# Kernel optimization log

Hardware: AMD Instinct MI355X
Metric: run time of the kernel (lower is better)

## Reference

```python
import jax, jax.numpy as jnp
import numpy as np

B, L = 32, 200
NUM_C, NUM_D, DIM_V = 256, 32, 128


def setup_inputs() -> dict:
    key = jax.random.key(0)
    ks = jax.random.split(key, 20)
    def n(k, shape, s=0.05):
        return (jax.random.normal(k, shape) * s).astype(jnp.float32)
    return {
        "c_seq": jax.random.randint(ks[0], (B, L), 0, NUM_C),
        "d_seq": jax.random.randint(ks[1], (B, L), 0, NUM_D),
        "r_seq": jax.random.uniform(ks[2], (B, L), dtype=jnp.float32),
        # learned params
        "X": n(ks[3], (NUM_C * NUM_D, DIM_V), 0.1),      # Embedding table
        "v_r": n(ks[4], (DIM_V,), 0.1),
        "v_beta": n(ks[5], (DIM_V,), 0.1),
        # GRU (torch layout: gates [r|z|n] stacked)
        "W_ih": n(ks[6], (3 * DIM_V, 2 * DIM_V)),
        "W_hh": n(ks[7], (3 * DIM_V, DIM_V)),
        "b_ih": n(ks[8], (3 * DIM_V,)),
        "b_hh": n(ks[9], (3 * DIM_V,)),
        # linear_1: dim_v -> dim_v -> num_d (dropout = identity in eval)
        "W1a": n(ks[10], (DIM_V, DIM_V)), "b1a": n(ks[11], (DIM_V,)),
        "W1b": n(ks[12], (NUM_D, DIM_V)), "b1b": n(ks[13], (NUM_D,)),
        # linear_2: 3*dim_v -> dim_v -> num_d
        "W2a": n(ks[14], (DIM_V, 3 * DIM_V)), "b2a": n(ks[15], (DIM_V,)),
        "W2b": n(ks[16], (NUM_D, DIM_V)), "b2b": n(ks[17], (NUM_D,)),
    }


def reference(c_seq, d_seq, r_seq, X, v_r, v_beta, W_ih, W_hh, b_ih, b_hh,
              W1a, b1a, W1b, b1b, W2a, b2a, W2b, b2b):
    # embedding lookup: x = c + num_c * d
    v_x_seq = X[c_seq + NUM_C * d_seq]              # [B,L,V]
    v_r_seq = r_seq[..., None] * v_r                # [B,L,V]
    gru_in = jnp.concatenate([v_x_seq, v_r_seq], -1)  # [B,L,2V]

    # GRU (torch semantics), precompute input projections
    gx = jnp.einsum('blf,gf->blg', gru_in, W_ih) + b_ih  # [B,L,3V]

    def gru_step(h, gx_t):
        gh = h @ W_hh.T + b_hh
        xr, xz, xn = jnp.split(gx_t, 3, axis=-1)
        hr, hz, hn = jnp.split(gh, 3, axis=-1)
        r = jax.nn.sigmoid(xr + hr)
        z = jax.nn.sigmoid(xz + hz)
        n_ = jnp.tanh(xn + r * hn)
        h = (1.0 - z) * n_ + z * h
        return h, h

    h0 = jnp.zeros((B, DIM_V), dtype=gru_in.dtype)
    _, h_seq = jax.lax.scan(gru_step, h0, jnp.swapaxes(gx, 0, 1))
    h_seq = jnp.swapaxes(h_seq, 0, 1)               # [B,L,V]

    # linear_1 (dropout is identity at inference)
    alpha_seq = jax.nn.relu(h_seq @ W1a.T + b1a) @ W1b.T + b1b  # [B,L,num_d]

    # sequential memory update; one-hot gather/scatter expressed as true
    # gather C[b, c_t, d_t] and row scatter C[b, c_t, :] = new_c (same math)
    bidx = jnp.arange(B)

    def mem_step(C, inp):
        c_t, d_t, vx_t, vr_t = inp
        beta = C[bidx, c_t, d_t]                    # [B]
        v_beta_t = beta[:, None] * v_beta           # [B,V]
        zcat = jnp.concatenate([v_beta_t, vx_t, vr_t], -1)  # [B,3V]
        new_c = jax.nn.relu(zcat @ W2a.T + b2a) @ W2b.T + b2b  # [B,num_d]
        C = C.at[bidx, c_t].set(new_c)
        return C, C

    C0 = jnp.zeros((B, NUM_C, NUM_D), jnp.float32)
    _, C_seq = jax.lax.scan(
        mem_step, C0,
        (jnp.swapaxes(c_seq, 0, 1), jnp.swapaxes(d_seq, 0, 1),
         jnp.swapaxes(v_x_seq, 0, 1), jnp.swapaxes(v_r_seq, 0, 1)))
    C_seq = jnp.swapaxes(C_seq, 0, 1)               # [B,L,num_c,num_d]
    return alpha_seq, h_seq, C_seq
```

## Files before the change

kernel.cpp:

```cpp
#include <hip/hip_runtime.h>
#include <hip/hip_bf16.h>

typedef unsigned short u16;
typedef unsigned int u32;
typedef short short8 __attribute__((ext_vector_type(8)));
typedef float f32x4 __attribute__((ext_vector_type(4)));

constexpr int BATCH = 32, L = 200, NUM_C = 256, NUM_D = 32, V = 128;
constexpr int G3 = 384;
constexpr int KQ = 512;
constexpr int ROWS = BATCH * L;
constexpr int TP = 208;
constexpr size_t ALPHA_OFF = 0;
constexpr size_t H_OFF = (size_t)ROWS * NUM_D;
constexpr size_t C_OFF = H_OFF + (size_t)ROWS * V;

__device__ inline u16 f2bf(float f) {
  __hip_bfloat16 h = __float2bfloat16(f);
  return __builtin_bit_cast(u16, h);
}
__device__ inline float bf2f(u16 u) { u32 x = ((u32)u) << 16; return __builtin_bit_cast(float, x); }

__device__ inline void cvt32(const float* __restrict__ src, u16* __restrict__ dst) {
#pragma unroll
  for (int j0 = 0; j0 < 32; j0 += 4) {
    const f32x4 v = *(const f32x4*)(src + j0);
    ushort4 s;
    s.x = f2bf(v[0]); s.y = f2bf(v[1]); s.z = f2bf(v[2]); s.w = f2bf(v[3]);
    *(ushort4*)(dst + j0) = s;
  }
}
__device__ inline short8 ldfrag(const float* __restrict__ p) {
  const f32x4 a = *(const f32x4*)p, b = *(const f32x4*)(p + 4);
  short8 s;
  s[0] = (short)f2bf(a[0]); s[1] = (short)f2bf(a[1]);
  s[2] = (short)f2bf(a[2]); s[3] = (short)f2bf(a[3]);
  s[4] = (short)f2bf(b[0]); s[5] = (short)f2bf(b[1]);
  s[6] = (short)f2bf(b[2]); s[7] = (short)f2bf(b[3]);
  return s;
}

__global__ __launch_bounds__(256) void k1(
    const int* __restrict__ c_seq, const int* __restrict__ d_seq,
    const float* __restrict__ r_seq, const float* __restrict__ X,
    const float* __restrict__ v_r, const float* __restrict__ W_ih,
    const float* __restrict__ W2a, const float* __restrict__ b_ih,
    const float* __restrict__ b2a, float* __restrict__ Qout)
{
  __shared__ __align__(16) u16 Als[64][144];
  __shared__ __align__(16) u16 Bls[64][144];
  const int tid = threadIdx.x;
  const int mt = blockIdx.x, nt = blockIdx.y;
  const int lane = tid & 63, w = tid >> 6;
  const int q = lane >> 4, m = lane & 15;

  f32x4 acc[4];
#pragma unroll
  for (int i = 0; i < 4; ++i) acc[i] = (f32x4)0.0f;

  const int r0 = tid >> 2;
  const int kc = (tid & 3) * 32;
  const int rowg = mt * 64 + r0;
  const int gcolB = nt * 64 + r0;

  for (int s = 0; s < 2; ++s) {
    if (s) __syncthreads();
    if (s == 0) {
      const int idx = c_seq[rowg] + NUM_C * d_seq[rowg];
      cvt32(X + (size_t)idx * V + kc, &Als[r0][kc]);
    } else {
      const float rv = r_seq[rowg];
#pragma unroll
      for (int j0 = 0; j0 < 32; j0 += 4) {
        const f32x4 v = *(const f32x4*)(v_r + kc + j0);
        ushort4 sv;
        sv.x = f2bf(rv * v[0]); sv.y = f2bf(rv * v[1]);
        sv.z = f2bf(rv * v[2]); sv.w = f2bf(rv * v[3]);
        *(ushort4*)&Als[r0][kc + j0] = sv;
      }
    }
    {
      const float* src = (gcolB < G3)
        ? (W_ih + (size_t)gcolB * 256 + s * 128 + kc)
        : (W2a + (size_t)(gcolB - G3) * G3 + V + s * 128 + kc);
      cvt32(src, &Bls[r0][kc]);
    }
    __syncthreads();
#pragma unroll
    for (int c = 0; c < 4; ++c) {
      const short8 af = *(const short8*)&Als[w * 16 + m][32 * c + 8 * q];
#pragma unroll
      for (int i = 0; i < 4; ++i) {
        const short8 bf = *(const short8*)&Bls[i * 16 + m][32 * c + 8 * q];
        acc[i] = __builtin_amdgcn_mfma_f32_16x16x32_bf16(af, bf, acc[i], 0, 0, 0);
      }
    }
  }
#pragma unroll
  for (int i = 0; i < 4; ++i) {
    const int col = nt * 64 + i * 16 + m;
    const float bias = (col < G3) ? b_ih[col] : b2a[col - G3];
#pragma unroll
    for (int r = 0; r < 4; ++r) {
      const int rowo = mt * 64 + w * 16 + q * 4 + r;
      Qout[(size_t)rowo * KQ + col] = acc[i][r] + bias;
    }
  }
}

union ShK2 {
  struct { u16 h_bf[2][V]; } g;
  struct {
    int cb[TP]; int db[TP]; int sp[TP];
    float nr[TP][36];
    float u[V];
    int maxd;
  } s;
};

__global__ __launch_bounds__(256, 1) void k2(
    const int* __restrict__ c_seq, const int* __restrict__ d_seq,
    const float* __restrict__ W_hh, const float* __restrict__ b_hh,
    const float* __restrict__ W2a, const float* __restrict__ v_beta,
    const float* __restrict__ W2b, const float* __restrict__ b2b,
    const float* __restrict__ Q, float* __restrict__ out)
{
  __shared__ __align__(16) ShK2 sh;
  const int tid = threadIdx.x;
  const int l = tid & 63, w = tid >> 6, q = l >> 4, m = l & 15;

  if (blockIdx.x < 32) {
    const int b = blockIdx.x;
    if (tid < V) sh.g.h_bf[0][tid] = 0;
    __syncthreads();
    short8 wf[6][4];
    float bhh[6]; int gcol[6];
#pragma unroll
    for (int i = 0; i < 6; ++i) {
      const int g = (w + 4 * i) * 16 + m;
      gcol[i] = g;
      bhh[i] = b_hh[g];
#pragma unroll
      for (int c = 0; c < 4; ++c)
        wf[i][c] = ldfrag(W_hh + (size_t)g * V + 32 * c + 8 * q);
    }
    const float* Qb = Q + (size_t)b * L * KQ;
    float* outh = out + H_OFF + (size_t)b * L * V;
    const int vi0 = 16 * w + m, vi1 = 64 + 16 * w + m;
    float hold[2] = {0.f, 0.f};
    float hst[2] = {0.f, 0.f};
    const f32x4 z4 = (f32x4)0.0f;
    float gxA[6], gxB[6];
#pragma unroll
    for (int i = 0; i < 6; ++i) gxA[i] = Qb[gcol[i]];
#pragma unroll
    for (int i = 0; i < 6; ++i) gxB[i] = Qb[KQ + gcol[i]];

    auto step = [&](int t, float (&gx)[6]) {
      const int rs = t & 1, wsl = rs ^ 1;
      short8 af[4];
#pragma unroll
      for (int c = 0; c < 4; ++c)
        af[c] = *(const short8*)&sh.g.h_bf[rs][32 * c + 8 * q];
      if (t > 0 && q == 0) {
        outh[(size_t)(t - 1) * V + vi0] = hst[0];
        outh[(size_t)(t - 1) * V + vi1] = hst[1];
      }
      f32x4 acc[6];
#pragma unroll
      for (int i = 0; i < 6; ++i)
        acc[i] = __builtin_amdgcn_mfma_f32_16x16x32_bf16(af[0], wf[i][0], z4, 0, 0, 0);
#pragma unroll
      for (int c = 1; c < 4; ++c)
#pragma unroll
        for (int i = 0; i < 6; ++i)
          acc[i] = __builtin_amdgcn_mfma_f32_16x16x32_bf16(af[c], wf[i][c], acc[i], 0, 0, 0);
      float hnew[2];
#pragma unroll
      for (int s = 0; s < 2; ++s) {
        const float xr = gx[0 + s] + acc[0 + s][0] + bhh[0 + s];
        const float xz = gx[2 + s] + acc[2 + s][0] + bhh[2 + s];
        const float ghn = acc[4 + s][0] + bhh[4 + s];
        const float r = 1.f / (1.f + __expf(-xr));
        const float z = 1.f / (1.f + __expf(-xz));
        const float xn = gx[4 + s] + r * ghn;
        const float e = __expf(2.f * xn);
        const float n = 1.f - 2.f / (e + 1.f);
        hnew[s] = (1.f - z) * n + z * hold[s];
      }
      if (q == 0) {
        sh.g.h_bf[wsl][vi0] = f2bf(hnew[0]);
        sh.g.h_bf[wsl][vi1] = f2bf(hnew[1]);
      }
      hold[0] = hnew[0]; hold[1] = hnew[1];
      hst[0] = hnew[0]; hst[1] = hnew[1];
      if (t + 2 < L) {
        const float* Qr = Qb + (size_t)(t + 2) * KQ;
#pragma unroll
        for (int i = 0; i < 6; ++i) gx[i] = Qr[gcol[i]];
      }
      __builtin_amdgcn_s_waitcnt(0xc07f);
      __builtin_amdgcn_s_barrier();
    };

    for (int t = 0; t < L; t += 2) {
      step(t, gxA);
      step(t + 1, gxB);
    }
    if (q == 0) {
      outh[(size_t)(L - 1) * V + vi0] = hst[0];
      outh[(size_t)(L - 1) * V + vi1] = hst[1];
    }
  } else {
    const int b = blockIdx.x - 32;
    for (int i = tid; i < TP; i += 256) {
      int c = -1, d = 0;
      if (i < L) { c = c_seq[b * L + i]; d = d_seq[b * L + i]; }
      sh.s.cb[i] = c; sh.s.db[i] = d; sh.s.sp[i] = -1;
    }
    if (tid < V) {
      float a = 0.f;
      const float* wr = W2a + (size_t)tid * G3;
      for (int k = 0; k < V; ++k) a += wr[k] * v_beta[k];
      sh.s.u[tid] = a;
    }
    if (tid == 0) sh.s.maxd = 0;
    __syncthreads();
    {
      const int c = tid;
      int prev = -1;
      for (int t4 = 0; t4 < L; t4 += 4) {
        const int4 v = *(const int4*)&sh.s.cb[t4];
        if (v.x == c) { sh.s.sp[t4 + 0] = prev; prev = t4 + 0; }
        if (v.y == c) { sh.s.sp[t4 + 1] = prev; prev = t4 + 1; }
        if (v.z == c) { sh.s.sp[t4 + 2] = prev; prev = t4 + 2; }
        if (v.w == c) { sh.s.sp[t4 + 3] = prev; prev = t4 + 3; }
      }
    }
    __syncthreads();
    {
      int dmx = 0;
      for (int t = tid; t < L; t += 256) {
        int dd = 0, s = sh.s.sp[t];
        while (s >= 0) { ++dd; s = sh.s.sp[s]; }
        dmx = dmx > dd ? dmx : dd;
      }
      atomicMax(&sh.s.maxd, dmx);
    }
    __syncthreads();
    const int rounds = sh.s.maxd + 1;
    float ureg[4][8];
#pragma unroll
    for (int c = 0; c < 4; ++c)
#pragma unroll
      for (int j = 0; j < 8; ++j) ureg[c][j] = sh.s.u[32 * c + 8 * q + j];
    short8 wbf[2][4];
    float bb[2];
#pragma unroll
    for (int tt = 0; tt < 2; ++tt) {
#pragma unroll
      for (int c = 0; c < 4; ++c)
        wbf[tt][c] = ldfrag(W2b + (size_t)(tt * 16 + m) * V + 32 * c + 8 * q);
      bb[tt] = b2b[tt * 16 + m];
    }
    const f32x4 z4 = (f32x4)0.0f;
    for (int rd = 0; rd < rounds; ++rd) {
      for (int ti = w; ti < 13; ti += 4) {
        const int t0 = ti * 16;
        const int tt = t0 + m;
        const bool ok = tt < L;
        const int spv = ok ? sh.s.sp[tt] : -1;
        const int dbv = ok ? sh.s.db[tt] : 0;
        const float beta = (spv >= 0) ? sh.s.nr[spv][dbv] : 0.f;
        const float* pr = Q + ((size_t)b * L + tt) * KQ + G3 + 8 * q;
        short8 af[4];
#pragma unroll
        for (int c = 0; c < 4; ++c) {
          const f32x4 p0 = ok ? *(const f32x4*)(pr + 32 * c) : (f32x4)0.0f;
          const f32x4 p1 = ok ? *(const f32x4*)(pr + 32 * c + 4) : (f32x4)0.0f;
          short8 a;
#pragma unroll
          for (int j = 0; j < 8; ++j) {
            const float pv = (j < 4) ? p0[j] : p1[j - 4];
            a[j] = (short)f2bf(fmaxf(beta * ureg[c][j] + pv, 0.f));
          }
          af[c] = a;
        }
        f32x4 a0 = z4, a1 = z4;
#pragma unroll
        for (int c = 0; c < 4; ++c) {
          a0 = __builtin_amdgcn_mfma_f32_16x16x32_bf16(af[c], wbf[0][c], a0, 0, 0, 0);
          a1 = __builtin_amdgcn_mfma_f32_16x16x32_bf16(af[c], wbf[1][c], a1, 0, 0, 0);
        }
#pragma unroll
        for (int r = 0; r < 4; ++r) {
          const int tr = t0 + q * 4 + r;
          sh.s.nr[tr][m]      = a0[r] + bb[0];
          sh.s.nr[tr][16 + m] = a1[r] + bb[1];
        }
      }
      __syncthreads();
    }
    float* outc = out + C_OFF + (size_t)b * L * (NUM_C * NUM_D);
    const int j4 = (tid & 7) * 4;
    for (int t = tid >> 3; t < L; t += 32) {
      const int c = sh.s.cb[t];
      float* oc = outc + (size_t)t * (NUM_C * NUM_D) + c * NUM_D + j4;
      *(f32x4*)oc = *(const f32x4*)&sh.s.nr[t][j4];
    }
  }
}

union ShK3 {
  struct { int cb[L]; float stage[L][NUM_D]; } f;
  struct { u16 hls[64][144]; u16 hid[64][144]; } a;
};

__global__ __launch_bounds__(256) void k3(
    const int* __restrict__ c_seq, const float* __restrict__ W1a,
    const float* __restrict__ b1a, const float* __restrict__ W1b,
    const float* __restrict__ b1b, float* __restrict__ out)
{
  __shared__ __align__(16) ShK3 sh;
  const int tid = threadIdx.x;
  if (blockIdx.x < 256) {
    const int blk = blockIdx.x;
    const int b = blk >> 3, cbase = (blk & 7) * 32;
    if (tid < L) sh.f.cb[tid] = c_seq[b * L + tid];
    __syncthreads();
    if (tid < L) {
      const int c = sh.f.cb[tid];
      if (c >= cbase && c < cbase + 32) {
        const float* src = out + C_OFF + ((size_t)b * L + tid) * (NUM_C * NUM_D) + (size_t)c * NUM_D;
#pragma unroll
        for (int j = 0; j < 8; ++j)
          *(f32x4*)&sh.f.stage[tid][j * 4] = *(const f32x4*)(src + j * 4);
      }
    }
    __syncthreads();
    const int cl = tid >> 3, dq = (tid & 7) * 4;
    const int myc = cbase + cl;
    float* base = out + C_OFF + (size_t)b * L * (NUM_C * NUM_D) + (size_t)myc * NUM_D + dq;
    f32x4 cur = (f32x4)0.0f;
    for (int t = 0; t < L; ++t) {
      if (sh.f.cb[t] == myc) cur = *(const f32x4*)&sh.f.stage[t][dq];
      *(f32x4*)base = cur;
      base += NUM_C * NUM_D;
    }
  } else {
    const int ab = blockIdx.x - 256;
    const int l = tid & 63, w = tid >> 6, q = l >> 4, m = l & 15;
    {
      const int r0 = tid >> 2, kc = (tid & 3) * 32;
      cvt32(out + H_OFF + (size_t)(ab * 64 + r0) * V + kc, &sh.a.hls[r0][kc]);
    }
    __syncthreads();
    f32x4 acc1[8];
#pragma unroll
    for (int i = 0; i < 8; ++i) acc1[i] = (f32x4)0.0f;
#pragma unroll
    for (int c = 0; c < 4; ++c) {
      const short8 af = *(const short8*)&sh.a.hls[w * 16 + m][32 * c + 8 * q];
#pragma unroll
      for (int i = 0; i < 8; ++i) {
        const short8 bf = ldfrag(W1a + (size_t)(i * 16 + m) * V + 32 * c + 8 * q);
        acc1[i] = __builtin_amdgcn_mfma_f32_16x16x32_bf16(af, bf, acc1[i], 0, 0, 0);
      }
    }
#pragma unroll
    for (int i = 0; i < 8; ++i) {
      const int col = i * 16 + m;
      const float bias = b1a[col];
#pragma unroll
      for (int r = 0; r < 4; ++r)
        sh.a.hid[w * 16 + q * 4 + r][col] = f2bf(fmaxf(acc1[i][r] + bias, 0.f));
    }
    __syncthreads();
    f32x4 acc2[2];
    acc2[0] = (f32x4)0.0f; acc2[1] = (f32x4)0.0f;
#pragma unroll
    for (int c = 0; c < 4; ++c) {
      const short8 af = *(const short8*)&sh.a.hid[w * 16 + m][32 * c + 8 * q];
#pragma unroll
      for (int tt = 0; tt < 2; ++tt) {
        const short8 bf = ldfrag(W1b + (size_t)(tt * 16 + m) * V + 32 * c + 8 * q);
        acc2[tt] = __builtin_amdgcn_mfma_f32_16x16x32_bf16(af, bf, acc2[tt], 0, 0, 0);
      }
    }
#pragma unroll
    for (int tt = 0; tt < 2; ++tt) {
      const int col = tt * 16 + m;
      const float bias = b1b[col];
#pragma unroll
      for (int r = 0; r < 4; ++r) {
        const int row = ab * 64 + w * 16 + q * 4 + r;
        out[ALPHA_OFF + (size_t)row * NUM_D + col] = acc2[tt][r] + bias;
      }
    }
  }
}

extern "C" void kernel_launch(void* const* d_in, const int* in_sizes, int n_in,
                              void* d_out, int out_size, void* d_ws, size_t ws_size,
                              hipStream_t stream) {
  const int*   c_seq  = (const int*)d_in[0];
  const int*   d_seq  = (const int*)d_in[1];
  const float* r_seq  = (const float*)d_in[2];
  const float* X      = (const float*)d_in[3];
  const float* v_r    = (const float*)d_in[4];
  const float* v_beta = (const float*)d_in[5];
  const float* W_ih   = (const float*)d_in[6];
  const float* W_hh   = (const float*)d_in[7];
  const float* b_ih   = (const float*)d_in[8];
  const float* b_hh   = (const float*)d_in[9];
  const float* W1a    = (const float*)d_in[10];
  const float* b1a    = (const float*)d_in[11];
  const float* W1b    = (const float*)d_in[12];
  const float* b1b    = (const float*)d_in[13];
  const float* W2a    = (const float*)d_in[14];
  const float* b2a    = (const float*)d_in[15];
  const float* W2b    = (const float*)d_in[16];
  const float* b2b    = (const float*)d_in[17];
  float* out = (float*)d_out;
  float* Q = (float*)d_ws;

  k1<<<dim3(100, 8), 256, 0, stream>>>(c_seq, d_seq, r_seq, X, v_r, W_ih, W2a, b_ih, b2a, Q);
  k2<<<64, 256, 0, stream>>>(c_seq, d_seq, W_hh, b_hh, W2a, v_beta, W2b, b2b, Q, out);
  k3<<<356, 256, 0, stream>>>(c_seq, W1a, b1a, W1b, b1b, out);
}
```

Before: 395.1 us.

## Fuse k2 and k3 into one launch with per-batch flag dependencies

Merges the GRU/memory kernel and the follow-up forward-fill and alpha kernels into a single launch of 420 blocks. Global counters and per-batch flags, reset in k1, let fill blocks start as soon as their batch's memory recurrence finishes, and let alpha blocks start once all GRU blocks finish. This removes a kernel boundary and overlaps the large C_seq fill writes with the tail of the recurrences. The cost is spin-waiting, which relies on producer blocks being scheduled before or alongside consumers, plus a lower occupancy hint of 2.

```diff
diff --git a/kernel.cpp b/kernel.cpp
--- a/kernel.cpp
+++ b/kernel.cpp
@@ -14,6 +14,9 @@
 constexpr size_t ALPHA_OFF = 0;
 constexpr size_t H_OFF = (size_t)ROWS * NUM_D;
 constexpr size_t C_OFF = H_OFF + (size_t)ROWS * V;
+
+__device__ int g_gcnt;
+__device__ int g_cflag[32];
 
 __device__ inline u16 f2bf(float f) {
   __hip_bfloat16 h = __float2bfloat16(f);
@@ -50,6 +53,11 @@
   __shared__ __align__(16) u16 Als[64][144];
   __shared__ __align__(16) u16 Bls[64][144];
   const int tid = threadIdx.x;
+  if (blockIdx.x == 0 && blockIdx.y == 0 && tid == 0) {
+    g_gcnt = 0;
+#pragma unroll
+    for (int i = 0; i < 32; ++i) g_cflag[i] = 0;
+  }
   const int mt = blockIdx.x, nt = blockIdx.y;
   const int lane = tid & 63, w = tid >> 6;
   const int q = lane >> 4, m = lane & 15;
@@ -108,7 +116,7 @@
   }
 }
 
-union ShK2 {
+union ShK23 {
   struct { u16 h_bf[2][V]; } g;
   struct {
     int cb[TP]; int db[TP]; int sp[TP];
@@ -116,21 +124,26 @@
     float u[V];
     int maxd;
   } s;
+  struct { int cb[L]; float stage[L][NUM_D]; } f;
+  struct { u16 hls[64][144]; u16 hid[64][144]; } a;
 };
 
-__global__ __launch_bounds__(256, 1) void k2(
+__global__ __launch_bounds__(256, 2) void k23(
     const int* __restrict__ c_seq, const int* __restrict__ d_seq,
     const float* __restrict__ W_hh, const float* __restrict__ b_hh,
     const float* __restrict__ W2a, const float* __restrict__ v_beta,
     const float* __restrict__ W2b, const float* __restrict__ b2b,
+    const float* __restrict__ W1a, const float* __restrict__ b1a,
+    const float* __restrict__ W1b, const float* __restrict__ b1b,
     const float* __restrict__ Q, float* __restrict__ out)
 {
-  __shared__ __align__(16) ShK2 sh;
+  __shared__ __align__(16) ShK23 sh;
   const int tid = threadIdx.x;
   const int l = tid & 63, w = tid >> 6, q = l >> 4, m = l & 15;
-
-  if (blockIdx.x < 32) {
-    const int b = blockIdx.x;
+  const int blk = blockIdx.x;
+
+  if (blk < 32) {
+    const int b = blk;
     if (tid < V) sh.g.h_bf[0][tid] = 0;
     __syncthreads();
     short8 wf[6][4];
@@ -211,8 +224,11 @@
       outh[(size_t)(L - 1) * V + vi0] = hst[0];
       outh[(size_t)(L - 1) * V + vi1] = hst[1];
     }
-  } else {
-    const int b = blockIdx.x - 32;
+    __threadfence();
+    __syncthreads();
+    if (tid == 0) atomicAdd(&g_gcnt, 1);
+  } else if (blk < 64) {
+    const int b = blk - 32;
     for (int i = tid; i < TP; i += 256) {
       int c = -1, d = 0;
       if (i < L) { c = c_seq[b * L + i]; d = d_seq[b * L + i]; }
@@ -308,26 +324,18 @@
       float* oc = outc + (size_t)t * (NUM_C * NUM_D) + c * NUM_D + j4;
       *(f32x4*)oc = *(const f32x4*)&sh.s.nr[t][j4];
     }
-  }
-}
-
-union ShK3 {
-  struct { int cb[L]; float stage[L][NUM_D]; } f;
-  struct { u16 hls[64][144]; u16 hid[64][144]; } a;
-};
-
-__global__ __launch_bounds__(256) void k3(
-    const int* __restrict__ c_seq, const float* __restrict__ W1a,
-    const float* __restrict__ b1a, const float* __restrict__ W1b,
-    const float* __restrict__ b1b, float* __restrict__ out)
-{
-  __shared__ __align__(16) ShK3 sh;
-  const int tid = threadIdx.x;
-  if (blockIdx.x < 256) {
-    const int blk = blockIdx.x;
-    const int b = blk >> 3, cbase = (blk & 7) * 32;
+    __threadfence();
+    __syncthreads();
+    if (tid == 0) atomicExch(&g_cflag[b], 1);
+  } else if (blk < 320) {
+    const int blk2 = blk - 64;
+    const int b = blk2 >> 3, cbase = (blk2 & 7) * 32;
     if (tid < L) sh.f.cb[tid] = c_seq[b * L + tid];
-    __syncthreads();
+    if (tid == 0) {
+      while (atomicAdd(&g_cflag[b], 0) == 0) __builtin_amdgcn_s_sleep(1);
+    }
+    __syncthreads();
+    __threadfence();
     if (tid < L) {
       const int c = sh.f.cb[tid];
       if (c >= cbase && c < cbase + 32) {
@@ -348,8 +356,12 @@
       base += NUM_C * NUM_D;
     }
   } else {
-    const int ab = blockIdx.x - 256;
-    const int l = tid & 63, w = tid >> 6, q = l >> 4, m = l & 15;
+    const int ab = blk - 320;
+    if (tid == 0) {
+      while (atomicAdd(&g_gcnt, 0) < 32) __builtin_amdgcn_s_sleep(1);
+    }
+    __syncthreads();
+    __threadfence();
     {
       const int r0 = tid >> 2, kc = (tid & 3) * 32;
       cvt32(out + H_OFF + (size_t)(ab * 64 + r0) * V + kc, &sh.a.hls[r0][kc]);
@@ -425,6 +437,6 @@
   float* Q = (float*)d_ws;
 
   k1<<<dim3(100, 8), 256, 0, stream>>>(c_seq, d_seq, r_seq, X, v_r, W_ih, W2a, b_ih, b2a, Q);
-  k2<<<64, 256, 0, stream>>>(c_seq, d_seq, W_hh, b_hh, W2a, v_beta, W2b, b2b, Q, out);
-  k3<<<356, 256, 0, stream>>>(c_seq, W1a, b1a, W1b, b1b, out);
-}
+  k23<<<420, 256, 0, stream>>>(c_seq, d_seq, W_hh, b_hh, W2a, v_beta, W2b, b2b,
+                               W1a, b1a, W1b, b1b, Q, out);
+}
```

After: 416.5 us. 5.4% more time.
